# Kernel optimization log

Hardware: AMD Instinct MI355X
Metric: run time of the kernel (lower is better)

The kernel has to match this reference:

```python
import jax, jax.numpy as jnp
import numpy as np

ROUTINGS = 3
EPS = 1e-7  # K.epsilon()

B, IN_CAPS, IN_DIM = 32, 2048, 16
NUM_CAPS, DIM_CAPS = 32, 16


def setup_inputs() -> dict:
    key = jax.random.key(0)
    k1, k2 = jax.random.split(key)
    x = jax.random.normal(k1, (B, IN_CAPS, IN_DIM), dtype=jnp.float32)
    # glorot-uniform-ish scale for capsule weights
    limit = np.sqrt(6.0 / (IN_DIM + DIM_CAPS)).astype(np.float32)
    W = jax.random.uniform(k2, (1, IN_CAPS, NUM_CAPS, DIM_CAPS, IN_DIM),
                           dtype=jnp.float32, minval=-limit, maxval=limit)
    return {"x": x, "W": W}


def _squash(v, axis=-1):
    s = jnp.sum(v * v, axis=axis, keepdims=True)
    scale = s / (1.0 + s) / jnp.sqrt(s + EPS)
    return scale * v


def reference(x, W):
    # inputs_hat[b,i,n,d] = sum_k W[0,i,n,d,k] * x[b,i,k]
    u = jnp.einsum('indk,bik->bind', W[0], x)  # [B, in_caps, num_caps, dim_caps]
    b = jnp.zeros(u.shape[:3], dtype=u.dtype)  # routing logits [B, in_caps, num_caps]
    outputs = None
    for i in range(ROUTINGS):
        c = jax.nn.softmax(b, axis=2)               # over num_capsule
        weighted = u * c[..., None]                 # [B, in, num, dim]
        outputs = _squash(jnp.sum(weighted, axis=1))  # [B, num, dim]
        if i < ROUTINGS - 1:
            # faithful to source: b += sum_d inputs_hat * c (NOT agreement with outputs)
            b = b + jnp.sum(weighted, axis=-1)
    return outputs
```

## Files before the change

### kernel.cpp

```cpp
#include <hip/hip_runtime.h>
#include <cstdint>
#include <cstddef>

#define LOG2E 1.4426950408889634f

template<int CTRL>
__device__ __forceinline__ float dpp_addf(float v) {
  const int s = __builtin_amdgcn_update_dpp(
      0, __builtin_bit_cast(int, v), CTRL, 0xF, 0xF, true);
  return v + __builtin_bit_cast(float, s);
}
#define DPP_XOR1     0xB1
#define DPP_XOR2     0x4E
#define DPP_HALF_MIR 0x141
#define DPP_ROW_MIR  0x140

__device__ __forceinline__ float rlane(float v, int l) {
  return __builtin_bit_cast(float,
      __builtin_amdgcn_readlane(__builtin_bit_cast(int, v), l));
}

__device__ __forceinline__ void gld_lds16(const float* g, float* l) {
  __builtin_amdgcn_global_load_lds(
      (const __attribute__((address_space(1))) void*)g,
      (__attribute__((address_space(3))) void*)l, 16, 0, 0);
}

__device__ __forceinline__ int swz(int b) { return b ^ ((b >> 3) & 7); }

__device__ __forceinline__ void stage_half(const float* Wg, float* buf,
                                           int wv, int ln) {
  #pragma unroll
  for (int t = 0; t < 2; ++t) {
    const int seg = ((wv << 1) + t) << 8;
    const int j   = swz((seg >> 2) + ln);
    gld_lds16(Wg + ((j >> 1) << 4) + ((j & 1) << 2), buf + seg);
  }
}

__device__ __forceinline__ void stage_tile(const float* WtI, float* buf,
                                           int wv, int ln) {
  stage_half(WtI,     buf,        wv, ln);
  stage_half(WtI + 8, buf + 4096, wv, ln);
}

__device__ __forceinline__ void stage_x(const float* Xi, float* dst, int tid) {
  if (tid < 128) {
    gld_lds16(Xi + ((size_t)(tid >> 2) << 15) + ((tid & 3) << 2),
              dst + ((tid >> 6) << 8));
  }
}

__device__ __forceinline__ void lds_barrier() {
  asm volatile("s_waitcnt lgkmcnt(0)\n\ts_barrier" ::: "memory");
}

template<bool ATOMIC>
__global__ __launch_bounds__(512)
void caps_main(const float* __restrict__ X, const float* __restrict__ Wt,
               float* __restrict__ part) {
  __shared__ float sW[8192];
  __shared__ float sX[2][512];
  __shared__ float sWs[32 * 20];
  __shared__ float sC[32 * 36];
  __shared__ float sPad[2688];
  if ((int)blockIdx.x == -1) sPad[threadIdx.x] = 1.f;

  const int tid  = threadIdx.x;
  const int wv   = tid >> 6, ln = tid & 63;
  const int t256 = tid & 255;
  const int bh   = tid >> 8;
  const int i0   = blockIdx.x << 2;

  stage_tile(Wt + ((size_t)i0 << 13), sW, wv, ln);
  stage_x(X + ((size_t)i0 << 4), sX[0], tid);

  const int bB = tid >> 4;
  const int n1 = tid & 15;
  const int j0 = t256 << 2;
  const int nr = t256 >> 3;

  float acc0[16], acc1[16];
  #pragma unroll
  for (int b = 0; b < 16; ++b) { acc0[b] = 0.f; acc1[b] = 0.f; }

  #pragma clang loop unroll(disable)
  for (int ii = 0; ii < 4; ++ii) {
    const int p = ii & 1;
    __syncthreads();

    const float4 wa0 = *(const float4*)&sW[swz(j0 + 0) << 2];
    const float4 wa1 = *(const float4*)&sW[swz(j0 + 1) << 2];
    const float4 wb0 = *(const float4*)&sW[swz(j0 + 2) << 2];
    const float4 wb1 = *(const float4*)&sW[swz(j0 + 3) << 2];
    const float4 wa2 = *(const float4*)&sW[4096 + (swz(j0 + 0) << 2)];
    const float4 wa3 = *(const float4*)&sW[4096 + (swz(j0 + 1) << 2)];
    const float4 wb2 = *(const float4*)&sW[4096 + (swz(j0 + 2) << 2)];
    const float4 wb3 = *(const float4*)&sW[4096 + (swz(j0 + 3) << 2)];

    const float4 xv = *(const float4*)
        &sX[p][(bh << 8) + ((ln >> 2) << 4) + ((ln & 3) << 2)];

    {
      const bool hi = tid >= 256;
      float pr[8];
      if (!hi) {
        pr[0]=wa0.x+wb0.x; pr[1]=wa0.y+wb0.y; pr[2]=wa0.z+wb0.z; pr[3]=wa0.w+wb0.w;
        pr[4]=wa1.x+wb1.x; pr[5]=wa1.y+wb1.y; pr[6]=wa1.z+wb1.z; pr[7]=wa1.w+wb1.w;
      } else {
        pr[0]=wa2.x+wb2.x; pr[1]=wa2.y+wb2.y; pr[2]=wa2.z+wb2.z; pr[3]=wa2.w+wb2.w;
        pr[4]=wa3.x+wb3.x; pr[5]=wa3.y+wb3.y; pr[6]=wa3.z+wb3.z; pr[7]=wa3.w+wb3.w;
      }
      #pragma unroll
      for (int q = 0; q < 8; ++q) {
        float v = pr[q];
        v = dpp_addf<DPP_XOR1>(v);
        v = dpp_addf<DPP_XOR2>(v);
        v = dpp_addf<DPP_HALF_MIR>(v);
        pr[q] = v;
      }
      const int m7 = tid & 7;
      const int mb = hi ? 2 : 0;
      if (m7 == mb || m7 == mb + 1) {
        const float4 w = (m7 == mb)
            ? make_float4(pr[0], pr[1], pr[2], pr[3])
            : make_float4(pr[4], pr[5], pr[6], pr[7]);
        *(float4*)&sWs[(t256 >> 3) * 20 + (m7 << 2)] = w;
      }
    }

    lds_barrier();

    if (ii < 3) {
      stage_x(X + ((size_t)(i0 + ii + 1) << 4), sX[p ^ 1], tid);
      stage_tile(Wt + ((size_t)(i0 + ii + 1) << 13), sW, wv, ln);
    }

    {
      const float* xr = &sX[p][bB << 4];
      const float4 x0 = *(const float4*)(xr + 0);
      const float4 x1 = *(const float4*)(xr + 4);
      const float4 x2 = *(const float4*)(xr + 8);
      const float4 x3 = *(const float4*)(xr + 12);
      float t1 = 0.f, t2 = 0.f;
      #pragma unroll
      for (int c4 = 0; c4 < 4; ++c4) {
        const float4 A1 = *(const float4*)&sWs[n1 * 20 + (c4 << 2)];
        const float4 A2 = *(const float4*)&sWs[(n1 + 16) * 20 + (c4 << 2)];
        const float4 xc = (c4 == 0) ? x0 : (c4 == 1) ? x1 : (c4 == 2) ? x2 : x3;
        t1 += A1.x * xc.x + A1.y * xc.y + A1.z * xc.z + A1.w * xc.w;
        t2 += A2.x * xc.x + A2.y * xc.y + A2.z * xc.z + A2.w * xc.w;
      }
      const float l1a = t1 * 0.03125f, l1b = t2 * 0.03125f;
      const float e1a = exp2f(l1a * LOG2E), e1b = exp2f(l1b * LOG2E);
      float s1 = e1a + e1b;
      s1 = dpp_addf<DPP_XOR1>(s1); s1 = dpp_addf<DPP_XOR2>(s1);
      s1 = dpp_addf<DPP_HALF_MIR>(s1); s1 = dpp_addf<DPP_ROW_MIR>(s1);
      const float rs1 = __builtin_amdgcn_rcpf(s1);
      const float l2a = l1a + e1a * rs1 * t1;
      const float l2b = l1b + e1b * rs1 * t2;
      const float e2a = exp2f(l2a * LOG2E), e2b = exp2f(l2b * LOG2E);
      float s2 = e2a + e2b;
      s2 = dpp_addf<DPP_XOR1>(s2); s2 = dpp_addf<DPP_XOR2>(s2);
      s2 = dpp_addf<DPP_HALF_MIR>(s2); s2 = dpp_addf<DPP_ROW_MIR>(s2);
      const float rs2 = __builtin_amdgcn_rcpf(s2);
      sC[n1 * 36 + bB]        = e2a * rs2;
      sC[(n1 + 16) * 36 + bB] = e2b * rs2;
    }

    float us0[8], us1[8];
    #pragma unroll
    for (int st = 0; st < 8; ++st) {
      if ((st & 3) == 0) __builtin_amdgcn_sched_barrier(0);
      const int lb = st << 2;
      const float s00 = rlane(xv.x, lb + 0), s01 = rlane(xv.y, lb + 0),
                  s02 = rlane(xv.z, lb + 0), s03 = rlane(xv.w, lb + 0);
      const float s10 = rlane(xv.x, lb + 1), s11 = rlane(xv.y, lb + 1),
                  s12 = rlane(xv.z, lb + 1), s13 = rlane(xv.w, lb + 1);
      const float s20 = rlane(xv.x, lb + 2), s21 = rlane(xv.y, lb + 2),
                  s22 = rlane(xv.z, lb + 2), s23 = rlane(xv.w, lb + 2);
      const float s30 = rlane(xv.x, lb + 3), s31 = rlane(xv.y, lb + 3),
                  s32 = rlane(xv.z, lb + 3), s33 = rlane(xv.w, lb + 3);
      us0[st] = wa0.x*s00 + wa0.y*s01 + wa0.z*s02 + wa0.w*s03
              + wa1.x*s10 + wa1.y*s11 + wa1.z*s12 + wa1.w*s13
              + wa2.x*s20 + wa2.y*s21 + wa2.z*s22 + wa2.w*s23
              + wa3.x*s30 + wa3.y*s31 + wa3.z*s32 + wa3.w*s33;
      us1[st] = wb0.x*s00 + wb0.y*s01 + wb0.z*s02 + wb0.w*s03
              + wb1.x*s10 + wb1.y*s11 + wb1.z*s12 + wb1.w*s13
              + wb2.x*s20 + wb2.y*s21 + wb2.z*s22 + wb2.w*s23
              + wb3.x*s30 + wb3.y*s31 + wb3.z*s32 + wb3.w*s33;
    }

    lds_barrier();

    float c2s[16];
    {
      const int cb = nr * 36 + (bh << 4);
      *(float4*)&c2s[0]  = *(const float4*)&sC[cb + 0];
      *(float4*)&c2s[4]  = *(const float4*)&sC[cb + 4];
      *(float4*)&c2s[8]  = *(const float4*)&sC[cb + 8];
      *(float4*)&c2s[12] = *(const float4*)&sC[cb + 12];
    }
    #pragma unroll
    for (int st = 0; st < 8; ++st) {
      acc0[st] += c2s[st] * us0[st];
      acc1[st] += c2s[st] * us1[st];
    }
    #pragma unroll
    for (int st = 8; st < 16; ++st) {
      if ((st & 3) == 0) __builtin_amdgcn_sched_barrier(0);
      const int lb = st << 2;
      const float s00 = rlane(xv.x, lb + 0), s01 = rlane(xv.y, lb + 0),
                  s02 = rlane(xv.z, lb + 0), s03 = rlane(xv.w, lb + 0);
      const float s10 = rlane(xv.x, lb + 1), s11 = rlane(xv.y, lb + 1),
                  s12 = rlane(xv.z, lb + 1), s13 = rlane(xv.w, lb + 1);
      const float s20 = rlane(xv.x, lb + 2), s21 = rlane(xv.y, lb + 2),
                  s22 = rlane(xv.z, lb + 2), s23 = rlane(xv.w, lb + 2);
      const float s30 = rlane(xv.x, lb + 3), s31 = rlane(xv.y, lb + 3),
                  s32 = rlane(xv.z, lb + 3), s33 = rlane(xv.w, lb + 3);
      float u0 = wa0.x*s00 + wa0.y*s01 + wa0.z*s02 + wa0.w*s03
               + wa1.x*s10 + wa1.y*s11 + wa1.z*s12 + wa1.w*s13
               + wa2.x*s20 + wa2.y*s21 + wa2.z*s22 + wa2.w*s23
               + wa3.x*s30 + wa3.y*s31 + wa3.z*s32 + wa3.w*s33;
      float u1 = wb0.x*s00 + wb0.y*s01 + wb0.z*s02 + wb0.w*s03
               + wb1.x*s10 + wb1.y*s11 + wb1.z*s12 + wb1.w*s13
               + wb2.x*s20 + wb2.y*s21 + wb2.z*s22 + wb2.w*s23
               + wb3.x*s30 + wb3.y*s31 + wb3.z*s32 + wb3.w*s33;
      acc0[st] += c2s[st] * u0;
      acc1[st] += c2s[st] * u1;
    }
  }

  if constexpr (ATOMIC) {
    #pragma unroll
    for (int j = 0; j < 16; ++j) {
      const int bgl = (bh << 4) + j;
      float* dst = part + ((size_t)bgl << 9) + (t256 << 1);
      atomicAdd(dst, acc0[j]);
      atomicAdd(dst + 1, acc1[j]);
    }
  } else {
    float* wp = part + ((size_t)blockIdx.x << 14) + (t256 << 1);
    #pragma unroll
    for (int j = 0; j < 16; ++j) {
      const int bgl = (bh << 4) + j;
      *(float2*)(wp + ((size_t)bgl << 9)) = make_float2(acc0[j], acc1[j]);
    }
  }
}

__global__ __launch_bounds__(512)
void caps_reduce(const float* __restrict__ part, float* __restrict__ out) {
  __shared__ float sred[32][64];
  const int tid = threadIdx.x;
  const int bid = blockIdx.x;
  const int b  = bid >> 3;
  const int rb = bid & 7;
  const int pg = tid >> 4;
  const int sl = tid & 15;
  const float* src = part + (((size_t)pg << 4) << 14)
                   + (b << 9) + (rb << 6) + (sl << 2);
  float4 a = make_float4(0.f, 0.f, 0.f, 0.f);
  #pragma unroll 4
  for (int p = 0; p < 16; ++p) {
    const float4 v = *(const float4*)(src + ((size_t)p << 14));
    a.x += v.x; a.y += v.y; a.z += v.z; a.w += v.w;
  }
  *(float4*)&sred[pg][sl << 2] = a;
  __syncthreads();
  if (tid < 64) {
    float s = 0.f;
    #pragma unroll
    for (int g = 0; g < 32; ++g) s += sred[g][tid];
    float sq = s * s;
    sq += __shfl_xor(sq, 1); sq += __shfl_xor(sq, 2);
    sq += __shfl_xor(sq, 4); sq += __shfl_xor(sq, 8);
    const float scale = sq / (1.0f + sq) / sqrtf(sq + 1e-7f);
    out[(b << 9) + (rb << 6) + tid] = scale * s;
  }
}

__global__ __launch_bounds__(256)
void caps_squash(const float* __restrict__ sums, float* __restrict__ out) {
  const int e = (blockIdx.x << 8) + threadIdx.x;
  const float s = sums[e];
  float sq = s * s;
  sq += __shfl_xor(sq, 1); sq += __shfl_xor(sq, 2);
  sq += __shfl_xor(sq, 4); sq += __shfl_xor(sq, 8);
  const float scale = sq / (1.0f + sq) / sqrtf(sq + 1e-7f);
  out[e] = scale * s;
}

extern "C" void kernel_launch(void* const* d_in, const int* in_sizes, int n_in,
                              void* d_out, int out_size, void* d_ws, size_t ws_size,
                              hipStream_t stream) {
  const float* X  = (const float*)d_in[0];
  const float* Wt = (const float*)d_in[1];
  float* out = (float*)d_out;
  float* wsf = (float*)d_ws;
  const size_t need = (size_t)512 * 16384 * sizeof(float);
  if (ws_size >= need) {
    caps_main<false><<<512, 512, 0, stream>>>(X, Wt, wsf);
    caps_reduce<<<256, 512, 0, stream>>>(wsf, out);
  } else {
    float* acc = (ws_size >= (size_t)16384 * sizeof(float)) ? wsf : out;
    hipMemsetAsync(acc, 0, 16384 * sizeof(float), stream);
    caps_main<true><<<512, 512, 0, stream>>>(X, Wt, acc);
    caps_squash<<<64, 256, 0, stream>>>(acc, out);
  }
}
```

Baseline: 44.56 us.

## Split batch halves across separate 256-thread blocks instead of one 512-thread block

The main kernel now launches 1024 blocks of 256 threads, with each block handling one half of the batch (16 samples) for a group of four input capsules, instead of 512 blocks of 512 threads covering both halves. The LDS padding array that throttled occupancy is removed and the X and softmax-coefficient buffers shrink to match. Each block now stages the full W tile on its own, so W traffic from global memory into LDS doubles, and each thread does the full 16-value shuffle reduction for the weight sums. The aim is more, smaller blocks for better occupancy and latency hiding, paid for with redundant W loads.

```diff
diff --git a/kernel.cpp b/kernel.cpp
--- a/kernel.cpp
+++ b/kernel.cpp
@@ -31,8 +31,8 @@
 __device__ __forceinline__ void stage_half(const float* Wg, float* buf,
                                            int wv, int ln) {
   #pragma unroll
-  for (int t = 0; t < 2; ++t) {
-    const int seg = ((wv << 1) + t) << 8;
+  for (int t = 0; t < 4; ++t) {
+    const int seg = ((wv << 2) + t) << 8;
     const int j   = swz((seg >> 2) + ln);
     gld_lds16(Wg + ((j >> 1) << 4) + ((j & 1) << 2), buf + seg);
   }
@@ -45,9 +45,8 @@
 }
 
 __device__ __forceinline__ void stage_x(const float* Xi, float* dst, int tid) {
-  if (tid < 128) {
-    gld_lds16(Xi + ((size_t)(tid >> 2) << 15) + ((tid & 3) << 2),
-              dst + ((tid >> 6) << 8));
+  if (tid < 64) {
+    gld_lds16(Xi + ((size_t)(tid >> 2) << 15) + ((tid & 3) << 2), dst);
   }
 }
 
@@ -56,29 +55,29 @@
 }
 
 template<bool ATOMIC>
-__global__ __launch_bounds__(512)
+__global__ __launch_bounds__(256)
 void caps_main(const float* __restrict__ X, const float* __restrict__ Wt,
                float* __restrict__ part) {
   __shared__ float sW[8192];
-  __shared__ float sX[2][512];
+  __shared__ float sX[2][256];
   __shared__ float sWs[32 * 20];
-  __shared__ float sC[32 * 36];
-  __shared__ float sPad[2688];
-  if ((int)blockIdx.x == -1) sPad[threadIdx.x] = 1.f;
+  __shared__ float sC[32 * 20];
 
   const int tid  = threadIdx.x;
   const int wv   = tid >> 6, ln = tid & 63;
-  const int t256 = tid & 255;
-  const int bh   = tid >> 8;
-  const int i0   = blockIdx.x << 2;
+  const int g    = blockIdx.x & 511;
+  const int h    = blockIdx.x >> 9;
+  const int i0   = g << 2;
+
+  const float* Xh = X + (((size_t)(h << 4)) << 15);
 
   stage_tile(Wt + ((size_t)i0 << 13), sW, wv, ln);
-  stage_x(X + ((size_t)i0 << 4), sX[0], tid);
+  stage_x(Xh + ((size_t)i0 << 4), sX[0], tid);
 
   const int bB = tid >> 4;
   const int n1 = tid & 15;
-  const int j0 = t256 << 2;
-  const int nr = t256 >> 3;
+  const int j0 = tid << 2;
+  const int nr = tid >> 3;
 
   float acc0[16], acc1[16];
   #pragma unroll
@@ -98,41 +97,36 @@
     const float4 wb2 = *(const float4*)&sW[4096 + (swz(j0 + 2) << 2)];
     const float4 wb3 = *(const float4*)&sW[4096 + (swz(j0 + 3) << 2)];
 
-    const float4 xv = *(const float4*)
-        &sX[p][(bh << 8) + ((ln >> 2) << 4) + ((ln & 3) << 2)];
+    const float4 xv = *(const float4*)&sX[p][ln << 2];
 
     {
-      const bool hi = tid >= 256;
-      float pr[8];
-      if (!hi) {
-        pr[0]=wa0.x+wb0.x; pr[1]=wa0.y+wb0.y; pr[2]=wa0.z+wb0.z; pr[3]=wa0.w+wb0.w;
-        pr[4]=wa1.x+wb1.x; pr[5]=wa1.y+wb1.y; pr[6]=wa1.z+wb1.z; pr[7]=wa1.w+wb1.w;
-      } else {
-        pr[0]=wa2.x+wb2.x; pr[1]=wa2.y+wb2.y; pr[2]=wa2.z+wb2.z; pr[3]=wa2.w+wb2.w;
-        pr[4]=wa3.x+wb3.x; pr[5]=wa3.y+wb3.y; pr[6]=wa3.z+wb3.z; pr[7]=wa3.w+wb3.w;
-      }
+      float pr[16] = { wa0.x+wb0.x, wa0.y+wb0.y, wa0.z+wb0.z, wa0.w+wb0.w,
+                       wa1.x+wb1.x, wa1.y+wb1.y, wa1.z+wb1.z, wa1.w+wb1.w,
+                       wa2.x+wb2.x, wa2.y+wb2.y, wa2.z+wb2.z, wa2.w+wb2.w,
+                       wa3.x+wb3.x, wa3.y+wb3.y, wa3.z+wb3.z, wa3.w+wb3.w };
       #pragma unroll
-      for (int q = 0; q < 8; ++q) {
+      for (int q = 0; q < 16; ++q) {
         float v = pr[q];
         v = dpp_addf<DPP_XOR1>(v);
         v = dpp_addf<DPP_XOR2>(v);
         v = dpp_addf<DPP_HALF_MIR>(v);
         pr[q] = v;
       }
-      const int m7 = tid & 7;
-      const int mb = hi ? 2 : 0;
-      if (m7 == mb || m7 == mb + 1) {
-        const float4 w = (m7 == mb)
-            ? make_float4(pr[0], pr[1], pr[2], pr[3])
-            : make_float4(pr[4], pr[5], pr[6], pr[7]);
-        *(float4*)&sWs[(t256 >> 3) * 20 + (m7 << 2)] = w;
+      if ((tid & 7) < 4) {
+        const int m = tid & 3;
+        const float4 w =
+            (m & 2) ? ((m & 1) ? make_float4(pr[12], pr[13], pr[14], pr[15])
+                               : make_float4(pr[8],  pr[9],  pr[10], pr[11]))
+                    : ((m & 1) ? make_float4(pr[4],  pr[5],  pr[6],  pr[7])
+                               : make_float4(pr[0],  pr[1],  pr[2],  pr[3]));
+        *(float4*)&sWs[(tid >> 3) * 20 + (m << 2)] = w;
       }
     }
 
     lds_barrier();
 
     if (ii < 3) {
-      stage_x(X + ((size_t)(i0 + ii + 1) << 4), sX[p ^ 1], tid);
+      stage_x(Xh + ((size_t)(i0 + ii + 1) << 4), sX[p ^ 1], tid);
       stage_tile(Wt + ((size_t)(i0 + ii + 1) << 13), sW, wv, ln);
     }
 
@@ -164,8 +158,8 @@
       s2 = dpp_addf<DPP_XOR1>(s2); s2 = dpp_addf<DPP_XOR2>(s2);
       s2 = dpp_addf<DPP_HALF_MIR>(s2); s2 = dpp_addf<DPP_ROW_MIR>(s2);
       const float rs2 = __builtin_amdgcn_rcpf(s2);
-      sC[n1 * 36 + bB]        = e2a * rs2;
-      sC[(n1 + 16) * 36 + bB] = e2b * rs2;
+      sC[n1 * 20 + bB]        = e2a * rs2;
+      sC[(n1 + 16) * 20 + bB] = e2b * rs2;
     }
 
     float us0[8], us1[8];
@@ -195,7 +189,7 @@
 
     float c2s[16];
     {
-      const int cb = nr * 36 + (bh << 4);
+      const int cb = nr * 20;
       *(float4*)&c2s[0]  = *(const float4*)&sC[cb + 0];
       *(float4*)&c2s[4]  = *(const float4*)&sC[cb + 4];
       *(float4*)&c2s[8]  = *(const float4*)&sC[cb + 8];
@@ -234,16 +228,16 @@
   if constexpr (ATOMIC) {
     #pragma unroll
     for (int j = 0; j < 16; ++j) {
-      const int bgl = (bh << 4) + j;
-      float* dst = part + ((size_t)bgl << 9) + (t256 << 1);
+      const int bgl = (h << 4) + j;
+      float* dst = part + ((size_t)bgl << 9) + (tid << 1);
       atomicAdd(dst, acc0[j]);
       atomicAdd(dst + 1, acc1[j]);
     }
   } else {
-    float* wp = part + ((size_t)blockIdx.x << 14) + (t256 << 1);
+    float* wp = part + ((size_t)g << 14) + (tid << 1);
     #pragma unroll
     for (int j = 0; j < 16; ++j) {
-      const int bgl = (bh << 4) + j;
+      const int bgl = (h << 4) + j;
       *(float2*)(wp + ((size_t)bgl << 9)) = make_float2(acc0[j], acc1[j]);
     }
   }
@@ -300,12 +294,12 @@
   float* wsf = (float*)d_ws;
   const size_t need = (size_t)512 * 16384 * sizeof(float);
   if (ws_size >= need) {
-    caps_main<false><<<512, 512, 0, stream>>>(X, Wt, wsf);
+    caps_main<false><<<1024, 256, 0, stream>>>(X, Wt, wsf);
     caps_reduce<<<256, 512, 0, stream>>>(wsf, out);
   } else {
     float* acc = (ws_size >= (size_t)16384 * sizeof(float)) ? wsf : out;
     hipMemsetAsync(acc, 0, 16384 * sizeof(float), stream);
-    caps_main<true><<<512, 512, 0, stream>>>(X, Wt, acc);
+    caps_main<true><<<1024, 256, 0, stream>>>(X, Wt, acc);
     caps_squash<<<64, 256, 0, stream>>>(acc, out);
   }
 }
```

Result: no change. 45.13 us (+1.3%).
